# Performance work log

Hardware: AMD Instinct MI355X
Metric: run time of the kernel (lower is better)

The kernel has to match this reference:

```python
import jax, jax.numpy as jnp
import numpy as np

B, S, DM, TD, H, HD = 2, 2048, 1024, 1024, 16, 64


def setup_inputs() -> dict:
    key = jax.random.key(0)
    k1, k2, k3, k4 = jax.random.split(key, 4)
    query = jax.random.normal(k1, (B, S, DM), dtype=jnp.float32)
    # fused QKV projection weight (nn.Linear weight layout: [out, in]) and output proj
    W_in = jax.random.normal(k2, (3 * TD, DM), dtype=jnp.float32) * 0.02
    W_out = jax.random.normal(k3, (DM, TD), dtype=jnp.float32) * 0.02
    # standard RoPE tables, broadcastable against [B, H, S, HD]
    inv_freq = 1.0 / (10000.0 ** (jnp.arange(0, HD, 2, dtype=jnp.float32) / HD))
    t = jnp.arange(S, dtype=jnp.float32)
    freqs = jnp.outer(t, inv_freq)                      # [S, HD/2]
    emb = jnp.concatenate([freqs, freqs], axis=-1)      # [S, HD]
    sin_q = jnp.sin(emb)[None, None]                    # [1,1,S,HD]
    cos_q = jnp.cos(emb)[None, None]
    # padding mask over keys: first length[b] positions valid (>= S/2 so no NaN rows)
    lengths = jax.random.randint(k4, (B,), S // 2, S + 1)
    attn_mask = jnp.arange(S)[None, :] < lengths[:, None]  # [B, S] bool
    return {"query": query, "W_in": W_in, "W_out": W_out,
            "sin_q": sin_q, "cos_q": cos_q, "attn_mask": attn_mask}


def _rotate_half(x):
    x1, x2 = jnp.split(x, 2, axis=-1)
    return jnp.concatenate([-x2, x1], axis=-1)


def reference(query, W_in, W_out, sin_q, cos_q, attn_mask):
    # fused QKV projection (proj_in, bias=False)
    qkv = query @ W_in.T                                # [B, S, 3*TD]
    q, k, v = jnp.split(qkv, 3, axis=-1)
    to_heads = lambda x: x.reshape(B, S, H, HD).transpose(0, 2, 1, 3)  # [B,H,S,HD]
    q, k, v = to_heads(q), to_heads(k), to_heads(v)
    # RoPE (prefix = 0 since sin covers full sequence)
    q = q * cos_q + _rotate_half(q) * sin_q
    k = k * cos_q + _rotate_half(k) * sin_q
    # SDPA with padding-mask bias + causal mask
    scale = 1.0 / jnp.sqrt(jnp.float32(HD))
    scores = jnp.einsum('bhqd,bhkd->bhqk', q, k) * scale  # [B,H,S,S]
    causal = jnp.arange(S)[:, None] >= jnp.arange(S)[None, :]  # [S, S]
    mask = attn_mask[:, None, None, :] & causal[None, None]    # [B,1,S,S]
    scores = jnp.where(mask, scores, -jnp.inf)
    attn = jax.nn.softmax(scores, axis=-1)
    out = jnp.einsum('bhqk,bhkd->bhqd', attn, v)        # [B,H,S,HD]
    out = out.transpose(0, 2, 1, 3).reshape(B, S, TD)
    return out @ W_out.T                                 # [B, S, DM]
```

## Files before the change

kernel.cpp:

```cpp
#include <hip/hip_runtime.h>
#include <hip/hip_bf16.h>

#define B_ 2
#define S_ 2048
#define DM_ 1024
#define TD_ 1024
#define H_ 16
#define HD_ 64

using bf16 = __hip_bfloat16;
typedef __attribute__((ext_vector_type(8))) short s8v;
typedef __attribute__((ext_vector_type(4))) float f4v;

__device__ __forceinline__ f4v mfma_bf16(s8v a, s8v b, f4v c) {
    return __builtin_amdgcn_mfma_f32_16x16x32_bf16(a, b, c, 0, 0, 0);
}

__device__ __forceinline__ unsigned cvt_pk_bf16(float a, float b) {
    unsigned r;
    asm("v_cvt_pk_bf16_f32 %0, %1, %2" : "=v"(r) : "v"(a), "v"(b));
    return r;
}
__device__ __forceinline__ int2 pack4bf(float a, float b, float c, float d) {
    int2 r;
    r.x = (int)cvt_pk_bf16(a, b);
    r.y = (int)cvt_pk_bf16(c, d);
    return r;
}

__device__ __forceinline__ bool detect_f32(const unsigned int* __restrict__ cosw) {
    return (cosw[0] & 0xFFFFu) == 0u;
}

__device__ __forceinline__ float ld_f(const void* p, int idx, bool f32) {
    return f32 ? ((const float*)p)[idx]
               : __bfloat162float(((const bf16*)p)[idx]);
}

__device__ __forceinline__ void gload_lds16(const bf16* g, void* l) {
    __builtin_amdgcn_global_load_lds(
        (const __attribute__((address_space(1))) unsigned int*)(const void*)g,
        (__attribute__((address_space(3))) unsigned int*)l,
        16, 0, 0);
}

#define NQ_  (B_ * S_ * DM_)
#define NWI_ (3 * TD_ * DM_)
#define NWO_ (DM_ * TD_)
#define NCVT_BLOCKS ((NQ_ + NWI_ + NWO_) / 2048)

__global__ __launch_bounds__(256)
void prep_all(const void* __restrict__ q, const void* __restrict__ wi,
              const void* __restrict__ wo, bf16* __restrict__ dst,
              const void* __restrict__ mask, int* __restrict__ lengths,
              const unsigned int* __restrict__ cosw) {
    const int bid = blockIdx.x;
    if (bid < NCVT_BLOCKS) {
        const bool f32 = detect_f32(cosw);
        int i = (bid * 256 + threadIdx.x) * 8;
        const void* src; int off;
        if (i < NQ_)              { src = q;  off = i; }
        else if (i < NQ_ + NWI_)  { src = wi; off = i - NQ_; }
        else                      { src = wo; off = i - NQ_ - NWI_; }
        if (f32) {
            const float* p = (const float*)src + off;
            float4 x = *reinterpret_cast<const float4*>(p);
            float4 y = *reinterpret_cast<const float4*>(p + 4);
            union { unsigned u[4]; int4 v; } t;
            t.u[0] = cvt_pk_bf16(x.x, x.y);
            t.u[1] = cvt_pk_bf16(x.z, x.w);
            t.u[2] = cvt_pk_bf16(y.x, y.y);
            t.u[3] = cvt_pk_bf16(y.z, y.w);
            *reinterpret_cast<int4*>(dst + i) = t.v;
        } else {
            *reinterpret_cast<int4*>(dst + i) =
                *reinterpret_cast<const int4*>((const bf16*)src + off);
        }
        return;
    }
    int b = bid - NCVT_BLOCKS;
    unsigned int w0 = ((const unsigned int*)mask)[0];
    int enc;
    if (w0 == 1u) enc = 0;
    else if (w0 == 0x01010101u) enc = 1;
    else if (w0 == 0x3F803F80u) enc = 2;
    else enc = 3;
    int cnt = 0;
    for (int s = threadIdx.x; s < S_; s += 256) {
        int i = b * S_ + s;
        bool v;
        if (enc == 0)      v = ((const int*)mask)[i] != 0;
        else if (enc == 1) v = ((const unsigned char*)mask)[i] != 0;
        else if (enc == 2) v = ((const unsigned short*)mask)[i] != 0;
        else               v = ((const float*)mask)[i] != 0.f;
        cnt += v ? 1 : 0;
    }
    __shared__ int red[256];
    red[threadIdx.x] = cnt;
    __syncthreads();
    for (int off = 128; off > 0; off >>= 1) {
        if (threadIdx.x < off) red[threadIdx.x] += red[threadIdx.x + off];
        __syncthreads();
    }
    if (threadIdx.x == 0) lengths[b] = red[0];
}

__global__ __launch_bounds__(256)
void gemm_nt(const bf16* __restrict__ A, const bf16* __restrict__ Bm,
             void* __restrict__ C, int M, int N, int K,
             int c_dyn, const unsigned int* __restrict__ cosw) {
    __shared__ bf16 lds_a[128 * 64];
    __shared__ bf16 lds_b[128 * 64];

    const bool cf32 = c_dyn && detect_f32(cosw);

    const int t = threadIdx.x;
    const int wave = t >> 6, lane = t & 63;
    const int quad = lane >> 4, l16 = lane & 15;
    const int wm = wave >> 1, wn = wave & 1;
    const int m0 = blockIdx.y * 128, n0 = blockIdx.x * 128;
    const int wuni = __builtin_amdgcn_readfirstlane(wave);

    f4v acc[4][4];
    #pragma unroll
    for (int i = 0; i < 4; i++)
        #pragma unroll
        for (int j = 0; j < 4; j++)
            acc[i][j] = f4v{0.f, 0.f, 0.f, 0.f};

    for (int k0 = 0; k0 < K; k0 += 64) {
        __syncthreads();
        #pragma unroll
        for (int i = 0; i < 4; i++) {
            int ci = i * 256 + t;
            int row = ci >> 3;
            int csrc = (ci & 7) ^ (row & 7);
            gload_lds16(A + (size_t)(m0 + row) * K + k0 + csrc * 8,
                        (char*)lds_a + i * 4096 + wuni * 1024);
            gload_lds16(Bm + (size_t)(n0 + row) * K + k0 + csrc * 8,
                        (char*)lds_b + i * 4096 + wuni * 1024);
        }
        __syncthreads();

        #pragma unroll
        for (int kk = 0; kk < 2; kk++) {
            s8v afr[4], bfr[4];
            #pragma unroll
            for (int mb = 0; mb < 4; mb++) {
                int r = wm * 64 + mb * 16 + l16;
                int ch = (kk * 4 + quad) ^ (l16 & 7);
                afr[mb] = *reinterpret_cast<const s8v*>(&lds_a[r * 64 + ch * 8]);
            }
            #pragma unroll
            for (int nb = 0; nb < 4; nb++) {
                int r = wn * 64 + nb * 16 + l16;
                int ch = (kk * 4 + quad) ^ (l16 & 7);
                bfr[nb] = *reinterpret_cast<const s8v*>(&lds_b[r * 64 + ch * 8]);
            }
            #pragma unroll
            for (int mb = 0; mb < 4; mb++)
                #pragma unroll
                for (int nb = 0; nb < 4; nb++)
                    acc[mb][nb] = mfma_bf16(bfr[nb], afr[mb], acc[mb][nb]);
        }
    }

    #pragma unroll
    for (int mb = 0; mb < 4; mb++) {
        int m = m0 + wm * 64 + mb * 16 + l16;
        #pragma unroll
        for (int nb = 0; nb < 4; nb++) {
            int n = n0 + wn * 64 + nb * 16 + quad * 4;
            f4v v = acc[mb][nb];
            if (cf32) {
                *reinterpret_cast<f4v*>(&((float*)C)[(size_t)m * N + n]) = v;
            } else {
                *reinterpret_cast<int2*>(&((bf16*)C)[(size_t)m * N + n]) =
                    pack4bf(v[0], v[1], v[2], v[3]);
            }
        }
    }
}

__global__ __launch_bounds__(256)
void rope_vt(const bf16* __restrict__ qkv,
             const void* __restrict__ sin_t, const void* __restrict__ cos_t,
             bf16* __restrict__ Qh, bf16* __restrict__ Kt, bf16* __restrict__ Vt) {
    __shared__ bf16 tile[64 * 72];
    const int bid = blockIdx.x;
    if (bid < 16384) {
        const bool f32 = detect_f32((const unsigned int*)cos_t);
        int idx = bid * 256 + threadIdx.x;
        int d = idx & 63;
        int h = (idx >> 6) & 15;
        int s = (idx >> 10) & 2047;
        int b = idx >> 21;
        size_t row = (size_t)(b * S_ + s) * 3072;
        int col  = h * 64 + d;
        int colp = h * 64 + ((d + 32) & 63);
        float sgn = (d < 32) ? -1.f : 1.f;
        float cs = ld_f(cos_t, s * 64 + d, f32);
        float sn = ld_f(sin_t, s * 64 + d, f32);
        float q  = __bfloat162float(qkv[row + col]);
        float qp = __bfloat162float(qkv[row + colp]);
        float k  = __bfloat162float(qkv[row + 1024 + col]);
        float kp = __bfloat162float(qkv[row + 1024 + colp]);
        Qh[((size_t)((b * H_ + h) * S_ + s)) * 64 + d] =
            __float2bfloat16((q * cs + sgn * qp * sn) * 0.180336880f);
        size_t ktile = ((size_t)(b * H_ + h) * 32 + (s >> 6)) * 4096;
        int dp = ((((d >> 3) ^ (s & 7)) << 3) | (d & 7));
        Kt[ktile + (s & 63) * 64 + dp] = __float2bfloat16(k * cs + sgn * kp * sn);
        return;
    }
    const int vid = bid - 16384;
    const int sb = vid & 31, h = (vid >> 5) & 15, b = vid >> 9;
    const int t = threadIdx.x;
    #pragma unroll
    for (int i = 0; i < 2; i++) {
        int id = i * 256 + t;
        int row = id >> 3, c = id & 7;
        *reinterpret_cast<int4*>(&tile[row * 72 + c * 8]) =
            *reinterpret_cast<const int4*>(
                qkv + (size_t)(b * S_ + sb * 64 + row) * 3072 + 2048 + h * 64 + c * 8);
    }
    __syncthreads();
    const size_t tb = ((size_t)(b * H_ + h) * 32 + sb) * 4096;
    #pragma unroll
    for (int i = 0; i < 2; i++) {
        int id = i * 256 + t;
        int d = id >> 3, kc = id & 7;
        union { short s[8]; int4 v; } u;
        #pragma unroll
        for (int e = 0; e < 8; e++)
            u.s[e] = reinterpret_cast<const short*>(tile)[(kc * 8 + e) * 72 + d];
        *reinterpret_cast<int4*>(Vt + tb + d * 64 + ((kc ^ (d & 7)) * 8)) = u.v;
    }
}

__global__ __launch_bounds__(256)
void attn_fused(const bf16* __restrict__ Qh, const bf16* __restrict__ Kt,
                const bf16* __restrict__ Vt, const int* __restrict__ lengths,
                bf16* __restrict__ out) {
    __shared__ bf16 k_buf[2 * 4096];
    __shared__ bf16 v_buf[2 * 4096];
    __shared__ bf16 lds_p[4 * 16 * 72];

    const int t = threadIdx.x, wave = t >> 6, lane = t & 63;
    const int quad = lane >> 4, l16 = lane & 15;
    const int bid = blockIdx.x;
    const int slot = bid >> 3;
    const int bh = (bid & 7) * 4 + (slot >> 4);
    const int p = slot & 15;
    const int b = bh >> 4, h = bh & 15;

    const size_t hb = (size_t)bh * S_ * 64;
    const bf16* Ktp = Kt + (size_t)bh * 32 * 4096;
    const bf16* Vtp = Vt + (size_t)bh * 32 * 4096;
    const int wuni = __builtin_amdgcn_readfirstlane(wave);
    int len_raw = lengths[b];
    const int len_b = len_raw < 1 ? 1 : (len_raw > S_ ? S_ : len_raw);
    const int nkt_len = (len_b + 63) >> 6;

    #pragma unroll
    for (int pass = 0; pass < 2; pass++) {
        const int qb = pass ? (31 - p) : p;
        const int qbase = qb * 64;
        const int qrow_g = qbase + wave * 16 + l16;
        const int kmax = (qrow_g < len_b - 1) ? qrow_g : (len_b - 1);

        s8v qf[2];
        {
            const bf16* qptr = Qh + hb + (size_t)qrow_g * 64 + quad * 8;
            qf[0] = *reinterpret_cast<const s8v*>(qptr);
            qf[1] = *reinterpret_cast<const s8v*>(qptr + 32);
        }

        f4v o_acc[4];
        #pragma unroll
        for (int a = 0; a < 4; a++) o_acc[a] = f4v{0.f, 0.f, 0.f, 0.f};
        float l_sum = 0.f;

        const int nkt = (qb + 1) < nkt_len ? (qb + 1) : nkt_len;

        f4v s_prev[4];
        auto process_tile = [&](int pt, const bf16* vb) {
            const int pbase = pt * 64;
            const bool tail = (pt == qb) || (pbase + 64 > len_b);
            #pragma unroll
            for (int a = 0; a < 4; a++) {
                float e0[4];
                #pragma unroll
                for (int r = 0; r < 4; r++) {
                    float e = __builtin_amdgcn_exp2f(s_prev[a][r]);
                    if (tail) {
                        int key = pbase + a * 16 + quad * 4 + r;
                        e = (key <= kmax) ? e : 0.f;
                    }
                    e0[r] = e;
                    l_sum += e;
                }
                *reinterpret_cast<int2*>(
                    &lds_p[(wave * 16 + l16) * 72 + a * 16 + quad * 4]) =
                    pack4bf(e0[0], e0[1], e0[2], e0[3]);
            }
            asm volatile("s_waitcnt lgkmcnt(0)" ::: "memory");
            #pragma unroll
            for (int kk = 0; kk < 2; kk++) {
                s8v pf = *reinterpret_cast<const s8v*>(
                    &lds_p[(wave * 16 + l16) * 72 + kk * 32 + quad * 8]);
                #pragma unroll
                for (int a = 0; a < 4; a++) {
                    int ch = (kk * 4 + quad) ^ (l16 & 7);
                    s8v vf = *reinterpret_cast<const s8v*>(
                        &vb[(a * 16 + l16) * 64 + ch * 8]);
                    o_acc[a] = mfma_bf16(vf, pf, o_acc[a]);
                }
            }
        };

        #pragma unroll
        for (int i = 0; i < 2; i++) {
            int ci = i * 256 + t;
            gload_lds16(Ktp + ci * 8, (char*)k_buf + i * 4096 + wuni * 1024);
        }
        __syncthreads();

        for (int kt = 0; kt < nkt; kt++) {
            const int cur = kt & 1;
            {
                const bf16* vst = Vtp + (size_t)kt * 4096;
                #pragma unroll
                for (int i = 0; i < 2; i++) {
                    int ci = i * 256 + t;
                    gload_lds16(vst + ci * 8,
                                (char*)v_buf + cur * 8192 + i * 4096 + wuni * 1024);
                }
            }
            if (kt + 1 < nkt) {
                const bf16* kst = Ktp + (size_t)(kt + 1) * 4096;
                #pragma unroll
                for (int i = 0; i < 2; i++) {
                    int ci = i * 256 + t;
                    gload_lds16(kst + ci * 8,
                                (char*)k_buf + (cur ^ 1) * 8192 + i * 4096 + wuni * 1024);
                }
            }

            const bf16* kb = k_buf + cur * 4096;
            f4v s_acc[4];
            #pragma unroll
            for (int a = 0; a < 4; a++) s_acc[a] = f4v{0.f, 0.f, 0.f, 0.f};
            #pragma unroll
            for (int kk = 0; kk < 2; kk++) {
                #pragma unroll
                for (int a = 0; a < 4; a++) {
                    int ch = (kk * 4 + quad) ^ (l16 & 7);
                    s8v kf = *reinterpret_cast<const s8v*>(
                        &kb[(a * 16 + l16) * 64 + ch * 8]);
                    s_acc[a] = mfma_bf16(kf, qf[kk], s_acc[a]);
                }
            }

            if (kt > 0) process_tile(kt - 1, v_buf + ((kt - 1) & 1) * 4096);

            #pragma unroll
            for (int a = 0; a < 4; a++) s_prev[a] = s_acc[a];

            __syncthreads();
        }
        process_tile(nkt - 1, v_buf + ((nkt - 1) & 1) * 4096);

        l_sum += __shfl_xor(l_sum, 16);
        l_sum += __shfl_xor(l_sum, 32);
        float inv_l = 1.f / l_sum;
        size_t orow = ((size_t)(b * S_ + qrow_g)) * TD_ + h * 64;
        #pragma unroll
        for (int a = 0; a < 4; a++) {
            *reinterpret_cast<int2*>(&out[orow + a * 16 + quad * 4]) =
                pack4bf(o_acc[a][0] * inv_l, o_acc[a][1] * inv_l,
                        o_acc[a][2] * inv_l, o_acc[a][3] * inv_l);
        }
    }
}

extern "C" void kernel_launch(void* const* d_in, const int* in_sizes, int n_in,
                              void* d_out, int out_size, void* d_ws, size_t ws_size,
                              hipStream_t stream) {
    const void* query = d_in[0];
    const void* W_in  = d_in[1];
    const void* W_out = d_in[2];
    const void* sin_q = d_in[3];
    const void* cos_q = d_in[4];
    const void* mask  = d_in[5];
    const unsigned int* cosw = (const unsigned int*)cos_q;

    const size_t nQ  = NQ_;
    const size_t nWi = NWI_;
    const size_t nWo = NWO_;

    bf16* qkv  = (bf16*)d_ws;
    bf16* Qh   = qkv + (size_t)4096 * 3072;
    bf16* Kt   = Qh + nQ;
    bf16* qbf  = Kt + nQ;
    bf16* wibf = qbf + nQ;
    bf16* wobf = wibf + nWi;
    int* lengths = (int*)(wobf + nWo);
    bf16* Vt   = qbf;
    bf16* attn = qkv;

    prep_all<<<NCVT_BLOCKS + B_, 256, 0, stream>>>(
        query, W_in, W_out, qbf, mask, lengths, cosw);

    dim3 g1(3072 / 128, 4096 / 128);
    gemm_nt<<<g1, 256, 0, stream>>>(qbf, wibf, qkv, 4096, 3072, 1024, 0, cosw);

    rope_vt<<<16384 + 1024, 256, 0, stream>>>(qkv, sin_q, cos_q, Qh, Kt, Vt);

    attn_fused<<<512, 256, 0, stream>>>(Qh, Kt, Vt, lengths, attn);

    dim3 g2(1024 / 128, 4096 / 128);
    gemm_nt<<<g2, 256, 0, stream>>>(attn, wobf, d_out, 4096, 1024, 1024, 1, cosw);
}
```

Before: 193.3 us.

## Process paired causal query blocks in one shared K/V loop

The attention kernel used to run two sequential passes per block, one for query block p and one for query block 31-p. It now runs a single K/V tile loop that computes both blocks at once, so K and V tiles 0..p are loaded into LDS once and serve both sets of MFMAs, and the second loop's prologue and syncs go away. The work-item mapping from block index to (head, p) is also changed so that p and its mirror are interleaved across slots. The cost is roughly double the live accumulators and score registers per wave, plus a second P buffer in LDS, which may lower occupancy.

```diff
diff --git a/kernel.cpp b/kernel.cpp
--- a/kernel.cpp
+++ b/kernel.cpp
@@ -243,14 +243,17 @@
                 bf16* __restrict__ out) {
     __shared__ bf16 k_buf[2 * 4096];
     __shared__ bf16 v_buf[2 * 4096];
-    __shared__ bf16 lds_p[4 * 16 * 72];
+    __shared__ bf16 lds_pA[4 * 16 * 72];
+    __shared__ bf16 lds_pB[4 * 16 * 72];
 
     const int t = threadIdx.x, wave = t >> 6, lane = t & 63;
     const int quad = lane >> 4, l16 = lane & 15;
     const int bid = blockIdx.x;
     const int slot = bid >> 3;
-    const int bh = (bid & 7) * 4 + (slot >> 4);
-    const int p = slot & 15;
+    const int s5 = slot & 31, hi = slot >> 5;
+    const int bh = (bid & 7) * 4 + (s5 & 3);
+    const int g = s5 >> 2;
+    const int p = hi ? (15 - g) : g;
     const int b = bh >> 4, h = bh & 15;
 
     const size_t hb = (size_t)bh * S_ * 64;
@@ -261,125 +264,156 @@
     const int len_b = len_raw < 1 ? 1 : (len_raw > S_ ? S_ : len_raw);
     const int nkt_len = (len_b + 63) >> 6;
 
-    #pragma unroll
-    for (int pass = 0; pass < 2; pass++) {
-        const int qb = pass ? (31 - p) : p;
-        const int qbase = qb * 64;
-        const int qrow_g = qbase + wave * 16 + l16;
-        const int kmax = (qrow_g < len_b - 1) ? qrow_g : (len_b - 1);
-
-        s8v qf[2];
+    const int qbA = p, qbB = 31 - p;
+    const int qrowA = qbA * 64 + wave * 16 + l16;
+    const int qrowB = qbB * 64 + wave * 16 + l16;
+    const int kmaxA = (qrowA < len_b - 1) ? qrowA : (len_b - 1);
+    const int kmaxB = (qrowB < len_b - 1) ? qrowB : (len_b - 1);
+
+    s8v qfA[2], qfB[2];
+    {
+        const bf16* qp_ = Qh + hb + (size_t)qrowA * 64 + quad * 8;
+        qfA[0] = *reinterpret_cast<const s8v*>(qp_);
+        qfA[1] = *reinterpret_cast<const s8v*>(qp_ + 32);
+        const bf16* qp2 = Qh + hb + (size_t)qrowB * 64 + quad * 8;
+        qfB[0] = *reinterpret_cast<const s8v*>(qp2);
+        qfB[1] = *reinterpret_cast<const s8v*>(qp2 + 32);
+    }
+
+    f4v oA[4], oB[4];
+    #pragma unroll
+    for (int a = 0; a < 4; a++) { oA[a] = f4v{0.f,0.f,0.f,0.f}; oB[a] = f4v{0.f,0.f,0.f,0.f}; }
+    float lA = 0.f, lB = 0.f;
+
+    const int nkt = (qbB + 1) < nkt_len ? (qbB + 1) : nkt_len;
+
+    f4v sA[4], sB[4];
+
+    auto process_prev = [&](int tau, bool actA, const bf16* vb) {
+        const int pbase = tau * 64;
+        const bool lenTail = (pbase + 64 > len_b);
         {
-            const bf16* qptr = Qh + hb + (size_t)qrow_g * 64 + quad * 8;
-            qf[0] = *reinterpret_cast<const s8v*>(qptr);
-            qf[1] = *reinterpret_cast<const s8v*>(qptr + 32);
-        }
-
-        f4v o_acc[4];
-        #pragma unroll
-        for (int a = 0; a < 4; a++) o_acc[a] = f4v{0.f, 0.f, 0.f, 0.f};
-        float l_sum = 0.f;
-
-        const int nkt = (qb + 1) < nkt_len ? (qb + 1) : nkt_len;
-
-        f4v s_prev[4];
-        auto process_tile = [&](int pt, const bf16* vb) {
-            const int pbase = pt * 64;
-            const bool tail = (pt == qb) || (pbase + 64 > len_b);
+            const bool tail = (tau == qbB) || lenTail;
             #pragma unroll
             for (int a = 0; a < 4; a++) {
                 float e0[4];
                 #pragma unroll
                 for (int r = 0; r < 4; r++) {
-                    float e = __builtin_amdgcn_exp2f(s_prev[a][r]);
+                    float e = __builtin_amdgcn_exp2f(sB[a][r]);
                     if (tail) {
                         int key = pbase + a * 16 + quad * 4 + r;
-                        e = (key <= kmax) ? e : 0.f;
+                        e = (key <= kmaxB) ? e : 0.f;
                     }
-                    e0[r] = e;
-                    l_sum += e;
+                    e0[r] = e; lB += e;
                 }
                 *reinterpret_cast<int2*>(
-                    &lds_p[(wave * 16 + l16) * 72 + a * 16 + quad * 4]) =
+                    &lds_pB[(wave * 16 + l16) * 72 + a * 16 + quad * 4]) =
                     pack4bf(e0[0], e0[1], e0[2], e0[3]);
             }
-            asm volatile("s_waitcnt lgkmcnt(0)" ::: "memory");
-            #pragma unroll
-            for (int kk = 0; kk < 2; kk++) {
-                s8v pf = *reinterpret_cast<const s8v*>(
-                    &lds_p[(wave * 16 + l16) * 72 + kk * 32 + quad * 8]);
+        }
+        if (actA) {
+            const bool tail = (tau == qbA) || lenTail;
+            #pragma unroll
+            for (int a = 0; a < 4; a++) {
+                float e0[4];
                 #pragma unroll
-                for (int a = 0; a < 4; a++) {
-                    int ch = (kk * 4 + quad) ^ (l16 & 7);
-                    s8v vf = *reinterpret_cast<const s8v*>(
-                        &vb[(a * 16 + l16) * 64 + ch * 8]);
-                    o_acc[a] = mfma_bf16(vf, pf, o_acc[a]);
+                for (int r = 0; r < 4; r++) {
+                    float e = __builtin_amdgcn_exp2f(sA[a][r]);
+                    if (tail) {
+                        int key = pbase + a * 16 + quad * 4 + r;
+                        e = (key <= kmaxA) ? e : 0.f;
+                    }
+                    e0[r] = e; lA += e;
                 }
-            }
-        };
-
-        #pragma unroll
-        for (int i = 0; i < 2; i++) {
-            int ci = i * 256 + t;
-            gload_lds16(Ktp + ci * 8, (char*)k_buf + i * 4096 + wuni * 1024);
-        }
+                *reinterpret_cast<int2*>(
+                    &lds_pA[(wave * 16 + l16) * 72 + a * 16 + quad * 4]) =
+                    pack4bf(e0[0], e0[1], e0[2], e0[3]);
+            }
+        }
+        asm volatile("s_waitcnt lgkmcnt(0)" ::: "memory");
+        #pragma unroll
+        for (int kk = 0; kk < 2; kk++) {
+            s8v pfB = *reinterpret_cast<const s8v*>(
+                &lds_pB[(wave * 16 + l16) * 72 + kk * 32 + quad * 8]);
+            s8v pfA;
+            if (actA) pfA = *reinterpret_cast<const s8v*>(
+                &lds_pA[(wave * 16 + l16) * 72 + kk * 32 + quad * 8]);
+            #pragma unroll
+            for (int a = 0; a < 4; a++) {
+                int ch = (kk * 4 + quad) ^ (l16 & 7);
+                s8v vf = *reinterpret_cast<const s8v*>(
+                    &vb[(a * 16 + l16) * 64 + ch * 8]);
+                oB[a] = mfma_bf16(vf, pfB, oB[a]);
+                if (actA) oA[a] = mfma_bf16(vf, pfA, oA[a]);
+            }
+        }
+    };
+
+    #pragma unroll
+    for (int i = 0; i < 2; i++) {
+        int ci = i * 256 + t;
+        gload_lds16(Ktp + ci * 8, (char*)k_buf + i * 4096 + wuni * 1024);
+    }
+    __syncthreads();
+
+    for (int kt = 0; kt < nkt; kt++) {
+        const int cur = kt & 1;
+        {
+            const bf16* vst = Vtp + (size_t)kt * 4096;
+            #pragma unroll
+            for (int i = 0; i < 2; i++) {
+                int ci = i * 256 + t;
+                gload_lds16(vst + ci * 8,
+                            (char*)v_buf + cur * 8192 + i * 4096 + wuni * 1024);
+            }
+        }
+        if (kt + 1 < nkt) {
+            const bf16* kst = Ktp + (size_t)(kt + 1) * 4096;
+            #pragma unroll
+            for (int i = 0; i < 2; i++) {
+                int ci = i * 256 + t;
+                gload_lds16(kst + ci * 8,
+                            (char*)k_buf + (cur ^ 1) * 8192 + i * 4096 + wuni * 1024);
+            }
+        }
+
+        const bf16* kb = k_buf + cur * 4096;
+        const bool actA_now = (kt <= p);
+        f4v s_nA[4], s_nB[4];
+        #pragma unroll
+        for (int a = 0; a < 4; a++) { s_nA[a] = f4v{0.f,0.f,0.f,0.f}; s_nB[a] = f4v{0.f,0.f,0.f,0.f}; }
+        #pragma unroll
+        for (int kk = 0; kk < 2; kk++) {
+            #pragma unroll
+            for (int a = 0; a < 4; a++) {
+                int ch = (kk * 4 + quad) ^ (l16 & 7);
+                s8v kf = *reinterpret_cast<const s8v*>(
+                    &kb[(a * 16 + l16) * 64 + ch * 8]);
+                s_nB[a] = mfma_bf16(kf, qfB[kk], s_nB[a]);
+                if (actA_now) s_nA[a] = mfma_bf16(kf, qfA[kk], s_nA[a]);
+            }
+        }
+
+        if (kt > 0) process_prev(kt - 1, (kt - 1) <= p, v_buf + ((kt - 1) & 1) * 4096);
+
+        #pragma unroll
+        for (int a = 0; a < 4; a++) { sB[a] = s_nB[a]; if (actA_now) sA[a] = s_nA[a]; }
+
         __syncthreads();
-
-        for (int kt = 0; kt < nkt; kt++) {
-            const int cur = kt & 1;
-            {
-                const bf16* vst = Vtp + (size_t)kt * 4096;
-                #pragma unroll
-                for (int i = 0; i < 2; i++) {
-                    int ci = i * 256 + t;
-                    gload_lds16(vst + ci * 8,
-                                (char*)v_buf + cur * 8192 + i * 4096 + wuni * 1024);
-                }
-            }
-            if (kt + 1 < nkt) {
-                const bf16* kst = Ktp + (size_t)(kt + 1) * 4096;
-                #pragma unroll
-                for (int i = 0; i < 2; i++) {
-                    int ci = i * 256 + t;
-                    gload_lds16(kst + ci * 8,
-                                (char*)k_buf + (cur ^ 1) * 8192 + i * 4096 + wuni * 1024);
-                }
-            }
-
-            const bf16* kb = k_buf + cur * 4096;
-            f4v s_acc[4];
-            #pragma unroll
-            for (int a = 0; a < 4; a++) s_acc[a] = f4v{0.f, 0.f, 0.f, 0.f};
-            #pragma unroll
-            for (int kk = 0; kk < 2; kk++) {
-                #pragma unroll
-                for (int a = 0; a < 4; a++) {
-                    int ch = (kk * 4 + quad) ^ (l16 & 7);
-                    s8v kf = *reinterpret_cast<const s8v*>(
-                        &kb[(a * 16 + l16) * 64 + ch * 8]);
-                    s_acc[a] = mfma_bf16(kf, qf[kk], s_acc[a]);
-                }
-            }
-
-            if (kt > 0) process_tile(kt - 1, v_buf + ((kt - 1) & 1) * 4096);
-
-            #pragma unroll
-            for (int a = 0; a < 4; a++) s_prev[a] = s_acc[a];
-
-            __syncthreads();
-        }
-        process_tile(nkt - 1, v_buf + ((nkt - 1) & 1) * 4096);
-
-        l_sum += __shfl_xor(l_sum, 16);
-        l_sum += __shfl_xor(l_sum, 32);
-        float inv_l = 1.f / l_sum;
-        size_t orow = ((size_t)(b * S_ + qrow_g)) * TD_ + h * 64;
-        #pragma unroll
-        for (int a = 0; a < 4; a++) {
-            *reinterpret_cast<int2*>(&out[orow + a * 16 + quad * 4]) =
-                pack4bf(o_acc[a][0] * inv_l, o_acc[a][1] * inv_l,
-                        o_acc[a][2] * inv_l, o_acc[a][3] * inv_l);
-        }
+    }
+    process_prev(nkt - 1, (nkt - 1) <= p, v_buf + ((nkt - 1) & 1) * 4096);
+
+    lA += __shfl_xor(lA, 16); lA += __shfl_xor(lA, 32);
+    lB += __shfl_xor(lB, 16); lB += __shfl_xor(lB, 32);
+    float invA = 1.f / lA, invB = 1.f / lB;
+    size_t orowA = ((size_t)(b * S_ + qrowA)) * TD_ + h * 64;
+    size_t orowB = ((size_t)(b * S_ + qrowB)) * TD_ + h * 64;
+    #pragma unroll
+    for (int a = 0; a < 4; a++) {
+        *reinterpret_cast<int2*>(&out[orowA + a * 16 + quad * 4]) =
+            pack4bf(oA[a][0] * invA, oA[a][1] * invA, oA[a][2] * invA, oA[a][3] * invA);
+        *reinterpret_cast<int2*>(&out[orowB + a * 16 + quad * 4]) =
+            pack4bf(oB[a][0] * invB, oB[a][1] * invB, oB[a][2] * invB, oB[a][3] * invB);
     }
 }
 
```

New measurement: 207.8 us. 1.08x slower.

## Process two KV tiles per barrier with a four-slot LDS ring buffer

Applied to the files above, without the earlier changes.

Grows the K and V shared-memory staging from double to quad buffers and unrolls the attention loop to handle two 64-key tiles per iteration. This halves the number of __syncthreads barriers and lets loads run further ahead of compute. In exchange, LDS use per block roughly doubles, which may lower occupancy, and the staging and ring indexing become more involved.

```diff
diff --git a/kernel.cpp b/kernel.cpp
--- a/kernel.cpp
+++ b/kernel.cpp
@@ -241,8 +241,8 @@
 void attn_fused(const bf16* __restrict__ Qh, const bf16* __restrict__ Kt,
                 const bf16* __restrict__ Vt, const int* __restrict__ lengths,
                 bf16* __restrict__ out) {
-    __shared__ bf16 k_buf[2 * 4096];
-    __shared__ bf16 v_buf[2 * 4096];
+    __shared__ bf16 k_buf[4 * 4096];
+    __shared__ bf16 v_buf[4 * 4096];
     __shared__ bf16 lds_p[4 * 16 * 72];
 
     const int t = threadIdx.x, wave = t >> 6, lane = t & 63;
@@ -261,6 +261,25 @@
     const int len_b = len_raw < 1 ? 1 : (len_raw > S_ ? S_ : len_raw);
     const int nkt_len = (len_b + 63) >> 6;
 
+    auto stageK = [&](int x) {
+        const bf16* src = Ktp + (size_t)x * 4096;
+        char* dstb = (char*)k_buf + (x & 3) * 8192;
+        #pragma unroll
+        for (int i = 0; i < 2; i++) {
+            int ci = i * 256 + t;
+            gload_lds16(src + ci * 8, dstb + i * 4096 + wuni * 1024);
+        }
+    };
+    auto stageV = [&](int x) {
+        const bf16* src = Vtp + (size_t)x * 4096;
+        char* dstb = (char*)v_buf + (x & 3) * 8192;
+        #pragma unroll
+        for (int i = 0; i < 2; i++) {
+            int ci = i * 256 + t;
+            gload_lds16(src + ci * 8, dstb + i * 4096 + wuni * 1024);
+        }
+    };
+
     #pragma unroll
     for (int pass = 0; pass < 2; pass++) {
         const int qb = pass ? (31 - p) : p;
@@ -283,7 +302,8 @@
         const int nkt = (qb + 1) < nkt_len ? (qb + 1) : nkt_len;
 
         f4v s_prev[4];
-        auto process_tile = [&](int pt, const bf16* vb) {
+        auto process_tile = [&](int pt) {
+            const bf16* vb = v_buf + (pt & 3) * 4096;
             const int pbase = pt * 64;
             const bool tail = (pt == qb) || (pbase + 64 > len_b);
             #pragma unroll
@@ -317,39 +337,8 @@
                 }
             }
         };
-
-        #pragma unroll
-        for (int i = 0; i < 2; i++) {
-            int ci = i * 256 + t;
-            gload_lds16(Ktp + ci * 8, (char*)k_buf + i * 4096 + wuni * 1024);
-        }
-        __syncthreads();
-
-        for (int kt = 0; kt < nkt; kt++) {
-            const int cur = kt & 1;
-            {
-                const bf16* vst = Vtp + (size_t)kt * 4096;
-                #pragma unroll
-                for (int i = 0; i < 2; i++) {
-                    int ci = i * 256 + t;
-                    gload_lds16(vst + ci * 8,
-                                (char*)v_buf + cur * 8192 + i * 4096 + wuni * 1024);
-                }
-            }
-            if (kt + 1 < nkt) {
-                const bf16* kst = Ktp + (size_t)(kt + 1) * 4096;
-                #pragma unroll
-                for (int i = 0; i < 2; i++) {
-                    int ci = i * 256 + t;
-                    gload_lds16(kst + ci * 8,
-                                (char*)k_buf + (cur ^ 1) * 8192 + i * 4096 + wuni * 1024);
-                }
-            }
-
-            const bf16* kb = k_buf + cur * 4096;
-            f4v s_acc[4];
-            #pragma unroll
-            for (int a = 0; a < 4; a++) s_acc[a] = f4v{0.f, 0.f, 0.f, 0.f};
+        auto smfma = [&](int x, f4v* sd) {
+            const bf16* kb = k_buf + (x & 3) * 4096;
             #pragma unroll
             for (int kk = 0; kk < 2; kk++) {
                 #pragma unroll
@@ -357,18 +346,46 @@
                     int ch = (kk * 4 + quad) ^ (l16 & 7);
                     s8v kf = *reinterpret_cast<const s8v*>(
                         &kb[(a * 16 + l16) * 64 + ch * 8]);
-                    s_acc[a] = mfma_bf16(kf, qf[kk], s_acc[a]);
+                    sd[a] = mfma_bf16(kf, qf[kk], sd[a]);
                 }
             }
-
-            if (kt > 0) process_tile(kt - 1, v_buf + ((kt - 1) & 1) * 4096);
-
-            #pragma unroll
-            for (int a = 0; a < 4; a++) s_prev[a] = s_acc[a];
+        };
+
+        __syncthreads();
+        stageK(0);
+        if (1 < nkt) stageK(1);
+        stageV(0);
+        __syncthreads();
+
+        const int n2 = (nkt + 1) >> 1;
+        for (int j = 0; j < n2; j++) {
+            const int t0 = 2 * j, t1 = t0 + 1;
+            if (t0 + 2 < nkt) stageK(t0 + 2);
+            if (t1 + 2 < nkt) stageK(t1 + 2);
+            if (t0 + 1 < nkt) stageV(t0 + 1);
+            if (t0 + 2 < nkt) stageV(t0 + 2);
+
+            f4v sn[4];
+            #pragma unroll
+            for (int a = 0; a < 4; a++) sn[a] = f4v{0.f, 0.f, 0.f, 0.f};
+            smfma(t0, sn);
+            if (j > 0) process_tile(t0 - 1);
+            #pragma unroll
+            for (int a = 0; a < 4; a++) s_prev[a] = sn[a];
+
+            if (t1 < nkt) {
+                f4v sn2[4];
+                #pragma unroll
+                for (int a = 0; a < 4; a++) sn2[a] = f4v{0.f, 0.f, 0.f, 0.f};
+                smfma(t1, sn2);
+                process_tile(t0);
+                #pragma unroll
+                for (int a = 0; a < 4; a++) s_prev[a] = sn2[a];
+            }
 
             __syncthreads();
         }
-        process_tile(nkt - 1, v_buf + ((nkt - 1) & 1) * 4096);
+        process_tile(nkt - 1);
 
         l_sum += __shfl_xor(l_sum, 16);
         l_sum += __shfl_xor(l_sum, 32);
```

After: 199.0 us. +3.0%, slower.

## Share K/V tiles across two adjacent query blocks per 512-thread workgroup

Applied to the files above, without the earlier changes.

The attention kernel now runs 512 threads per block, with two groups of four waves each handling an adjacent 64-row query block. Both groups share one staged K/V tile stream, replacing the earlier scheme where each block processed a query block and its mirror in two sequential passes. This roughly halves K/V global-to-LDS traffic per query row and removes the serial second pass. In exchange, the group with the lower block idles during the last key tile, block scheduling is remapped for causal load balance, and register and LDS pressure per block rise, which may cut occupancy.

```diff
diff --git a/kernel.cpp b/kernel.cpp
--- a/kernel.cpp
+++ b/kernel.cpp
@@ -237,20 +237,32 @@
     }
 }
 
-__global__ __launch_bounds__(256)
+__global__ __launch_bounds__(512)
 void attn_fused(const bf16* __restrict__ Qh, const bf16* __restrict__ Kt,
                 const bf16* __restrict__ Vt, const int* __restrict__ lengths,
                 bf16* __restrict__ out) {
     __shared__ bf16 k_buf[2 * 4096];
     __shared__ bf16 v_buf[2 * 4096];
-    __shared__ bf16 lds_p[4 * 16 * 72];
+    __shared__ bf16 lds_p[8 * 16 * 72];
 
     const int t = threadIdx.x, wave = t >> 6, lane = t & 63;
     const int quad = lane >> 4, l16 = lane & 15;
+    const int grp = wave >> 2;
+    const int wq = wave & 3;
+
     const int bid = blockIdx.x;
-    const int slot = bid >> 3;
-    const int bh = (bid & 7) * 4 + (slot >> 4);
-    const int p = slot & 15;
+    const int xcd = bid & 7;
+    int g, bh;
+    if (bid < 256) {
+        int r = bid >> 3;
+        bh = xcd * 4 + (r & 3);
+        g = r >> 2;
+    } else {
+        int r = (bid - 256) >> 3;
+        bh = xcd * 4 + (r & 3);
+        g = 15 - (r >> 2);
+    }
+    const int qb = 2 * g + grp;
     const int b = bh >> 4, h = bh & 15;
 
     const size_t hb = (size_t)bh * S_ * 64;
@@ -261,95 +273,83 @@
     const int len_b = len_raw < 1 ? 1 : (len_raw > S_ ? S_ : len_raw);
     const int nkt_len = (len_b + 63) >> 6;
 
-    #pragma unroll
-    for (int pass = 0; pass < 2; pass++) {
-        const int qb = pass ? (31 - p) : p;
-        const int qbase = qb * 64;
-        const int qrow_g = qbase + wave * 16 + l16;
-        const int kmax = (qrow_g < len_b - 1) ? qrow_g : (len_b - 1);
-
-        s8v qf[2];
-        {
-            const bf16* qptr = Qh + hb + (size_t)qrow_g * 64 + quad * 8;
-            qf[0] = *reinterpret_cast<const s8v*>(qptr);
-            qf[1] = *reinterpret_cast<const s8v*>(qptr + 32);
-        }
-
-        f4v o_acc[4];
-        #pragma unroll
-        for (int a = 0; a < 4; a++) o_acc[a] = f4v{0.f, 0.f, 0.f, 0.f};
-        float l_sum = 0.f;
-
-        const int nkt = (qb + 1) < nkt_len ? (qb + 1) : nkt_len;
-
-        f4v s_prev[4];
-        auto process_tile = [&](int pt, const bf16* vb) {
-            const int pbase = pt * 64;
-            const bool tail = (pt == qb) || (pbase + 64 > len_b);
+    const int nkt_w = (qb + 1) < nkt_len ? (qb + 1) : nkt_len;
+    const int nkt   = (2 * g + 2) < nkt_len ? (2 * g + 2) : nkt_len;
+
+    const int qrow_g = qb * 64 + wq * 16 + l16;
+    const int kmax = (qrow_g < len_b - 1) ? qrow_g : (len_b - 1);
+
+    s8v qf[2];
+    {
+        const bf16* qptr = Qh + hb + (size_t)qrow_g * 64 + quad * 8;
+        qf[0] = *reinterpret_cast<const s8v*>(qptr);
+        qf[1] = *reinterpret_cast<const s8v*>(qptr + 32);
+    }
+
+    f4v o_acc[4];
+    #pragma unroll
+    for (int a = 0; a < 4; a++) o_acc[a] = f4v{0.f, 0.f, 0.f, 0.f};
+    float l_sum = 0.f;
+
+    auto stageK = [&](int x) {
+        gload_lds16(Ktp + (size_t)x * 4096 + t * 8,
+                    (char*)k_buf + (x & 1) * 8192 + wuni * 1024);
+    };
+    auto stageV = [&](int x) {
+        gload_lds16(Vtp + (size_t)x * 4096 + t * 8,
+                    (char*)v_buf + (x & 1) * 8192 + wuni * 1024);
+    };
+
+    f4v s_prev[4];
+    auto process_tile = [&](int pt) {
+        const bf16* vb = v_buf + (pt & 1) * 4096;
+        const int pbase = pt * 64;
+        const bool tail = (pt == qb) || (pbase + 64 > len_b);
+        #pragma unroll
+        for (int a = 0; a < 4; a++) {
+            float e0[4];
+            #pragma unroll
+            for (int r = 0; r < 4; r++) {
+                float e = __builtin_amdgcn_exp2f(s_prev[a][r]);
+                if (tail) {
+                    int key = pbase + a * 16 + quad * 4 + r;
+                    e = (key <= kmax) ? e : 0.f;
+                }
+                e0[r] = e;
+                l_sum += e;
+            }
+            *reinterpret_cast<int2*>(
+                &lds_p[(wave * 16 + l16) * 72 + a * 16 + quad * 4]) =
+                pack4bf(e0[0], e0[1], e0[2], e0[3]);
+        }
+        asm volatile("s_waitcnt lgkmcnt(0)" ::: "memory");
+        #pragma unroll
+        for (int kk = 0; kk < 2; kk++) {
+            s8v pf = *reinterpret_cast<const s8v*>(
+                &lds_p[(wave * 16 + l16) * 72 + kk * 32 + quad * 8]);
             #pragma unroll
             for (int a = 0; a < 4; a++) {
-                float e0[4];
-                #pragma unroll
-                for (int r = 0; r < 4; r++) {
-                    float e = __builtin_amdgcn_exp2f(s_prev[a][r]);
-                    if (tail) {
-                        int key = pbase + a * 16 + quad * 4 + r;
-                        e = (key <= kmax) ? e : 0.f;
-                    }
-                    e0[r] = e;
-                    l_sum += e;
-                }
-                *reinterpret_cast<int2*>(
-                    &lds_p[(wave * 16 + l16) * 72 + a * 16 + quad * 4]) =
-                    pack4bf(e0[0], e0[1], e0[2], e0[3]);
-            }
-            asm volatile("s_waitcnt lgkmcnt(0)" ::: "memory");
-            #pragma unroll
-            for (int kk = 0; kk < 2; kk++) {
-                s8v pf = *reinterpret_cast<const s8v*>(
-                    &lds_p[(wave * 16 + l16) * 72 + kk * 32 + quad * 8]);
-                #pragma unroll
-                for (int a = 0; a < 4; a++) {
-                    int ch = (kk * 4 + quad) ^ (l16 & 7);
-                    s8v vf = *reinterpret_cast<const s8v*>(
-                        &vb[(a * 16 + l16) * 64 + ch * 8]);
-                    o_acc[a] = mfma_bf16(vf, pf, o_acc[a]);
-                }
-            }
-        };
-
-        #pragma unroll
-        for (int i = 0; i < 2; i++) {
-            int ci = i * 256 + t;
-            gload_lds16(Ktp + ci * 8, (char*)k_buf + i * 4096 + wuni * 1024);
-        }
-        __syncthreads();
-
-        for (int kt = 0; kt < nkt; kt++) {
-            const int cur = kt & 1;
-            {
-                const bf16* vst = Vtp + (size_t)kt * 4096;
-                #pragma unroll
-                for (int i = 0; i < 2; i++) {
-                    int ci = i * 256 + t;
-                    gload_lds16(vst + ci * 8,
-                                (char*)v_buf + cur * 8192 + i * 4096 + wuni * 1024);
-                }
-            }
-            if (kt + 1 < nkt) {
-                const bf16* kst = Ktp + (size_t)(kt + 1) * 4096;
-                #pragma unroll
-                for (int i = 0; i < 2; i++) {
-                    int ci = i * 256 + t;
-                    gload_lds16(kst + ci * 8,
-                                (char*)k_buf + (cur ^ 1) * 8192 + i * 4096 + wuni * 1024);
-                }
-            }
-
-            const bf16* kb = k_buf + cur * 4096;
-            f4v s_acc[4];
-            #pragma unroll
-            for (int a = 0; a < 4; a++) s_acc[a] = f4v{0.f, 0.f, 0.f, 0.f};
+                int ch = (kk * 4 + quad) ^ (l16 & 7);
+                s8v vf = *reinterpret_cast<const s8v*>(
+                    &vb[(a * 16 + l16) * 64 + ch * 8]);
+                o_acc[a] = mfma_bf16(vf, pf, o_acc[a]);
+            }
+        }
+    };
+
+    stageK(0);
+    __syncthreads();
+
+    for (int kt = 0; kt < nkt; kt++) {
+        stageV(kt);
+        if (kt + 1 < nkt) stageK(kt + 1);
+
+        const bool act = (kt < nkt_w);
+        f4v sn[4];
+        if (act) {
+            const bf16* kb = k_buf + (kt & 1) * 4096;
+            #pragma unroll
+            for (int a = 0; a < 4; a++) sn[a] = f4v{0.f, 0.f, 0.f, 0.f};
             #pragma unroll
             for (int kk = 0; kk < 2; kk++) {
                 #pragma unroll
@@ -357,29 +357,31 @@
                     int ch = (kk * 4 + quad) ^ (l16 & 7);
                     s8v kf = *reinterpret_cast<const s8v*>(
                         &kb[(a * 16 + l16) * 64 + ch * 8]);
-                    s_acc[a] = mfma_bf16(kf, qf[kk], s_acc[a]);
+                    sn[a] = mfma_bf16(kf, qf[kk], sn[a]);
                 }
             }
-
-            if (kt > 0) process_tile(kt - 1, v_buf + ((kt - 1) & 1) * 4096);
-
-            #pragma unroll
-            for (int a = 0; a < 4; a++) s_prev[a] = s_acc[a];
-
-            __syncthreads();
-        }
-        process_tile(nkt - 1, v_buf + ((nkt - 1) & 1) * 4096);
-
-        l_sum += __shfl_xor(l_sum, 16);
-        l_sum += __shfl_xor(l_sum, 32);
-        float inv_l = 1.f / l_sum;
-        size_t orow = ((size_t)(b * S_ + qrow_g)) * TD_ + h * 64;
-        #pragma unroll
-        for (int a = 0; a < 4; a++) {
-            *reinterpret_cast<int2*>(&out[orow + a * 16 + quad * 4]) =
-                pack4bf(o_acc[a][0] * inv_l, o_acc[a][1] * inv_l,
-                        o_acc[a][2] * inv_l, o_acc[a][3] * inv_l);
-        }
+        }
+
+        if (kt >= 1 && (kt - 1) < nkt_w) process_tile(kt - 1);
+
+        if (act) {
+            #pragma unroll
+            for (int a = 0; a < 4; a++) s_prev[a] = sn[a];
+        }
+
+        __syncthreads();
+    }
+    if (nkt_w == nkt) process_tile(nkt_w - 1);
+
+    l_sum += __shfl_xor(l_sum, 16);
+    l_sum += __shfl_xor(l_sum, 32);
+    float inv_l = 1.f / l_sum;
+    size_t orow = ((size_t)(b * S_ + qrow_g)) * TD_ + h * 64;
+    #pragma unroll
+    for (int a = 0; a < 4; a++) {
+        *reinterpret_cast<int2*>(&out[orow + a * 16 + quad * 4]) =
+            pack4bf(o_acc[a][0] * inv_l, o_acc[a][1] * inv_l,
+                    o_acc[a][2] * inv_l, o_acc[a][3] * inv_l);
     }
 }
 
@@ -416,7 +418,7 @@
 
     rope_vt<<<16384 + 1024, 256, 0, stream>>>(qkv, sin_q, cos_q, Qh, Kt, Vt);
 
-    attn_fused<<<512, 256, 0, stream>>>(Qh, Kt, Vt, lengths, attn);
+    attn_fused<<<512, 512, 0, stream>>>(Qh, Kt, Vt, lengths, attn);
 
     dim3 g2(1024 / 128, 4096 / 128);
     gemm_nt<<<g2, 256, 0, stream>>>(attn, wobf, d_out, 4096, 1024, 1024, 1, cosw);
```

After: 197.5 us. 1.02x slower.
